# Kernel optimization log

Hardware: AMD Instinct MI355X
Metric: run time of the kernel (lower is better)

## Reference

```python
import jax, jax.numpy as jnp
import numpy as np

N, E, B, BLOCK = 100000, 1600000, 8, 12500
IN, HID, K, OUT = 128, 128, 4, 2
EPS = 1e-15


def setup_inputs() -> dict:
    key = jax.random.key(0)
    ks = jax.random.split(key, 14)
    x = jax.random.normal(ks[0], (N, IN), jnp.float32)
    # edges constrained within each graph's contiguous node block
    src = jax.random.randint(ks[1], (E,), 0, N)
    off = jax.random.randint(ks[2], (E,), 0, BLOCK)
    dst = (src // BLOCK) * BLOCK + off
    edge_index = jnp.stack([src, dst])
    batch = jnp.arange(N) // BLOCK
    s = 0.02
    params = dict(
        W_root1=jax.random.normal(ks[3], (IN, HID), jnp.float32) * s,
        W_rel1=jax.random.normal(ks[4], (IN, HID), jnp.float32) * s,
        b_rel1=jnp.zeros((HID,), jnp.float32),
        W_pool=jax.random.normal(ks[5], (HID, K), jnp.float32) * s,
        b_pool=jnp.zeros((K,), jnp.float32),
        W_rel3=jax.random.normal(ks[6], (HID, HID), jnp.float32) * s,
        b_rel3=jnp.zeros((HID,), jnp.float32),
        W_root3=jax.random.normal(ks[7], (HID, HID), jnp.float32) * s,
        W_lin1=jax.random.normal(ks[8], (HID, HID), jnp.float32) * s,
        b_lin1=jnp.zeros((HID,), jnp.float32),
        W_lin2=jax.random.normal(ks[9], (HID, OUT), jnp.float32) * s,
        b_lin2=jnp.zeros((OUT,), jnp.float32),
    )
    return dict(x=x, edge_index=edge_index, batch=batch, **params)


def _forward(x, edge_index, batch, W_root1, W_rel1, b_rel1, W_pool, b_pool,
             W_rel3, b_rel3, W_root3, W_lin1, b_lin1, W_lin2, b_lin2):
    src, dst = edge_index[0], edge_index[1]
    # GraphConv (aggr='add'): lin_rel(sum_j x_j) + lin_root(x)
    agg = jax.ops.segment_sum(x[src], dst, num_segments=N)  # [N, IN]
    h = jax.nn.relu(agg @ W_rel1 + b_rel1 + x @ W_root1)    # [N, HID]
    # cluster assignment
    s = jax.nn.softmax(h @ W_pool + b_pool, axis=-1)        # [N, K]
    # pooled node features: out[b] = S_b^T X_b  -> [B, K, HID]
    out = jax.ops.segment_sum(s[:, :, None] * h[:, None, :], batch, num_segments=B)
    # coarsened adjacency: out_adj[b] = S_b^T A_b S_b (A[dst, src] = 1 per edge)
    e_graph = batch[dst]
    contrib = s[dst][:, :, None] * s[src][:, None, :]       # [E, K, K]
    out_adj = jax.ops.segment_sum(contrib, e_graph, num_segments=B)  # [B, K, K]
    # mincut loss
    mincut_num = jnp.einsum('bkk->b', out_adj)
    deg = jax.ops.segment_sum(jnp.ones((E,), x.dtype), dst, num_segments=N)
    mincut_den = jax.ops.segment_sum(deg * jnp.sum(s * s, axis=-1), batch, num_segments=B)
    mc_loss = jnp.mean(-(mincut_num / mincut_den))
    # orthogonality loss
    ss = jax.ops.segment_sum(s[:, :, None] * s[:, None, :], batch, num_segments=B)  # [B,K,K]
    ss_norm = jnp.linalg.norm(ss, axis=(1, 2), keepdims=True)
    i_s = jnp.eye(K, dtype=x.dtype)
    o_loss = jnp.mean(jnp.linalg.norm(ss / ss_norm - i_s / jnp.sqrt(jnp.float32(K)), axis=(1, 2)))
    # fix and normalize coarsened adjacency
    out_adj = out_adj * (1.0 - i_s)  # zero diagonal
    d = jnp.sqrt(jnp.sum(out_adj, axis=-1)) + EPS  # [B, K]
    out_adj = out_adj / d[:, None, :] / d[:, :, None]
    # DenseGraphConv (aggr='add'): lin_rel(adj @ x) + lin_root(x)
    x2 = jnp.einsum('bkl,blc->bkc', out_adj, out) @ W_rel3 + b_rel3 + out @ W_root3
    x2 = jnp.mean(x2, axis=1)  # [B, HID]
    x2 = jax.nn.relu(x2 @ W_lin1 + b_lin1)
    logits = x2 @ W_lin2 + b_lin2
    return jax.nn.log_softmax(logits, axis=-1), mc_loss, o_loss, s, out_adj


def reference(x, edge_index, batch, W_root1, W_rel1, b_rel1, W_pool, b_pool,
              W_rel3, b_rel3, W_root3, W_lin1, b_lin1, W_lin2, b_lin2):
    return _forward(x, edge_index, batch, W_root1, W_rel1, b_rel1, W_pool, b_pool,
                    W_rel3, b_rel3, W_root3, W_lin1, b_lin1, W_lin2, b_lin2)
```

## Files before the change

### kernel.cpp

```cpp
#include <hip/hip_runtime.h>

#define NN     100000
#define EE     1600000
#define NB     8
#define BLK    12500
#define HID    128
#define KC     4
#define CHUNKS 196
#define NTILE  49
#define NBIN   392
#define GCAPS  5120

typedef __attribute__((ext_vector_type(8))) short bf16x8;
typedef __attribute__((ext_vector_type(4))) float f32x4;

__device__ __forceinline__ ushort f2bf(float f) {
  uint u = __float_as_uint(f);
  return (ushort)((u + 0x7FFFu + ((u >> 16) & 1u)) >> 16);
}
__device__ __forceinline__ float bf2f(ushort h) {
  return __uint_as_float(((uint)h) << 16);
}

#define GLL16(g, l) \
  __builtin_amdgcn_global_load_lds((const __attribute__((address_space(1))) void*)(g), \
                                   (__attribute__((address_space(3))) void*)(l), 16, 0, 0)

__global__ __launch_bounds__(256) void k_prep(const float4* __restrict__ x4,
                                              ushort* __restrict__ xb,
                                              const float* __restrict__ Wrel1,
                                              const float* __restrict__ Wroot1,
                                              ushort* __restrict__ Wt,
                                              const int* __restrict__ ei,
                                              int* __restrict__ sbcnt,
                                              uint* __restrict__ gbuf) {
  __shared__ uint stage[8192];
  __shared__ int cnt[NBIN], start[NBIN + 1], rbase[NBIN];
  __shared__ int gtot[8], gb[8];
  const int bi = blockIdx.x;
  const int t = threadIdx.x;
  if (bi >= 196) {
    const int pb = bi - 196;
    if (pb < 12500) {
      int i = pb * 256 + t;
      float4 v = x4[i];
      ushort4 r;
      r.x = f2bf(v.x); r.y = f2bf(v.y); r.z = f2bf(v.z); r.w = f2bf(v.w);
      *(ushort4*)(xb + (size_t)i * 4) = r;
    } else {
      int col = pb - 12500, k = t;
      float v = (k < 128) ? Wrel1[k * 128 + col] : Wroot1[(k - 128) * 128 + col];
      Wt[col * 256 + k] = f2bf(v);
    }
    return;
  }
  for (int b = t; b < NBIN; b += 256) cnt[b] = 0;
  __syncthreads();
  const int e0 = bi * 8192;
  uint pk[32]; int br[32];
#pragma unroll
  for (int i = 0; i < 32; ++i) {
    int e = e0 + i * 256 + t;
    bool val = (e < EE);
    int src = 0, dst = 0;
    if (val) {
      src = __builtin_nontemporal_load(ei + e);
      dst = __builtin_nontemporal_load(ei + EE + e);
    }
    int g = dst / BLK;
    int dl = dst - g * BLK;
    int sl = src - g * BLK;
    int bin = g * NTILE + (dl >> 8);
    pk[i] = ((uint)sl << 16) | (uint)dl;
    br[i] = val ? ((bin << 14) | atomicAdd(&cnt[bin], 1)) : -1;
  }
  __syncthreads();
  if (t < 8) {
    int s = 0;
    for (int k = 0; k < NTILE; ++k) s += cnt[t * NTILE + k];
    gtot[t] = s;
  }
  __syncthreads();
  if (t == 0) {
    int s = 0;
    for (int g = 0; g < 8; ++g) { gb[g] = s; s += gtot[g]; }
    start[NBIN] = s;
  }
  __syncthreads();
  if (t < 8) {
    int run = gb[t];
    for (int k = 0; k < NTILE; ++k) { start[t * NTILE + k] = run; run += cnt[t * NTILE + k]; }
  }
  __syncthreads();
  for (int b = t; b < NBIN; b += 256) rbase[b] = atomicAdd(&sbcnt[b], cnt[b]);
#pragma unroll
  for (int i = 0; i < 32; ++i) {
    if (br[i] >= 0) {
      int bin = br[i] >> 14, rank = br[i] & 16383;
      stage[start[bin] + rank] = pk[i];
    }
  }
  __syncthreads();
  for (int b = t; b < NBIN; b += 256) {
    const int n = cnt[b];
    const int s0 = start[b];
    uint* dst = gbuf + (size_t)b * GCAPS + rbase[b];
    for (int i = 0; i < n; ++i) dst[i] = stage[s0 + i];
  }
}

__global__ __launch_bounds__(256) void k_csr_tile(const uint* __restrict__ gbuf,
                                                  const int* __restrict__ sbcnt,
                                                  int* __restrict__ rowptr,
                                                  int* __restrict__ count,
                                                  int* __restrict__ csr) {
  const int g = blockIdx.x & 7;
  const int tile = blockIdx.x >> 3;
  const int bin = g * NTILE + tile;
  const int m = sbcnt[bin];
  const int n0t = tile * 256;
  const int nt = min(256, BLK - n0t);
  __shared__ uint ent[GCAPS];
  __shared__ ushort srt[GCAPS];
  __shared__ int cnt[256], scn[256], cur[256];
  __shared__ int red[256];
  const int t = threadIdx.x;
  {
    int partial = 0;
    for (int i = t; i < bin; i += 256) partial += sbcnt[i];
    red[t] = partial;
    __syncthreads();
    for (int off = 128; off > 0; off >>= 1) {
      if (t < off) red[t] += red[t + off];
      __syncthreads();
    }
  }
  const int base = red[0];
  cnt[t] = 0;
  __syncthreads();
  const uint* buf = gbuf + (size_t)bin * GCAPS;
  for (int i = t; i < m; i += 256) {
    uint pk = buf[i];
    ent[i] = pk;
    atomicAdd(&cnt[(int)(pk & 0xFFFFu) - n0t], 1);
  }
  __syncthreads();
  int v = cnt[t];
  scn[t] = v;
  __syncthreads();
  for (int s = 1; s < 256; s <<= 1) {
    int x = (t >= s) ? scn[t - s] : 0;
    __syncthreads();
    scn[t] += x;
    __syncthreads();
  }
  int excl = scn[t] - v;
  cur[t] = excl;
  if (t < nt) {
    rowptr[g * BLK + n0t + t] = base + excl;
    count[g * BLK + n0t + t] = v;
  }
  __syncthreads();
  for (int i = t; i < m; i += 256) {
    uint pk = ent[i];
    int p = atomicAdd(&cur[(int)(pk & 0xFFFFu) - n0t], 1);
    srt[p] = (ushort)(pk >> 16);
  }
  __syncthreads();
  const int nb = g * BLK;
  for (int i = t; i < m; i += 256)
    csr[base + i] = nb + (int)srt[i];
}

__global__ __launch_bounds__(256) void k_agg2(const ushort* __restrict__ xb,
                                              const int* __restrict__ count,
                                              const int* __restrict__ rowptr,
                                              const int* __restrict__ csr,
                                              const ushort* __restrict__ zrow,
                                              ushort* __restrict__ aggb) {
  const int xg = blockIdx.x & 7;
  const int j = blockIdx.x >> 3;
  const int half = threadIdx.x >> 5;
  const int lane = threadIdx.x & 31;
  const int ln = j * 8 + half;
  if (ln >= BLK) return;
  const int node = xg * BLK + ln;
  const int deg = count[node];
  const int* sl = csr + rowptr[node];
  int idx0 = (lane < deg) ? sl[lane] : 0;
  int idx1 = (32 + lane < deg) ? sl[32 + lane] : 0;
  const ushort* zr = zrow + lane * 4;

  float4 acc[8];
#pragma unroll
  for (int q = 0; q < 8; ++q) acc[q] = (float4){0.f, 0.f, 0.f, 0.f};

  const int nb8 = (deg + 7) >> 3;
  for (int b = 0; b < nb8; ++b) {
    const int e = b * 8;
    const ushort* ps[8];
#pragma unroll
    for (int q = 0; q < 8; ++q) {
      int ee = e + q;
      int si = (ee < 32) ? __shfl(idx0, ee, 32)
             : ((ee < 64) ? __shfl(idx1, ee - 32, 32)
                          : ((ee < deg) ? sl[ee] : 0));
      ps[q] = (ee < deg) ? (xb + (size_t)si * HID + lane * 4) : zr;
    }
    uint2 v[8];
#pragma unroll
    for (int q = 0; q < 8; ++q) v[q] = *(const uint2*)ps[q];
#pragma unroll
    for (int q = 0; q < 8; ++q) {
      acc[q].x += __uint_as_float(v[q].x << 16);
      acc[q].y += __uint_as_float(v[q].x & 0xFFFF0000u);
      acc[q].z += __uint_as_float(v[q].y << 16);
      acc[q].w += __uint_as_float(v[q].y & 0xFFFF0000u);
    }
  }

  float lo0 = 0.f, hi0 = 0.f, lo1 = 0.f, hi1 = 0.f;
#pragma unroll
  for (int q = 0; q < 8; ++q) { lo0 += acc[q].x; hi0 += acc[q].y; lo1 += acc[q].z; hi1 += acc[q].w; }
  ushort4 r;
  r.x = f2bf(lo0); r.y = f2bf(hi0); r.z = f2bf(lo1); r.w = f2bf(hi1);
  *(ushort4*)(aggb + (size_t)node * HID + lane * 4) = r;
}

__global__ __launch_bounds__(256) void k_gemm(
    const ushort* __restrict__ aggb, const ushort* __restrict__ xb,
    const ushort* __restrict__ Wt, const float* __restrict__ brel1,
    const float* __restrict__ Wpool, const float* __restrict__ bpool,
    ushort* __restrict__ hbuf, float* __restrict__ s_out) {
  __shared__ ushort Aag_s[64][128];
  __shared__ ushort Ax_s[64][128];
  __shared__ ushort hLb[64][136];

  const int t = threadIdx.x;
  const int bi = blockIdx.x;
  const int bG = bi & 7;
  const int chunk = bi >> 3;
  const int node0 = bG * BLK + chunk * 64;
  int nrows = BLK - chunk * 64;
  if (nrows > 64) nrows = 64;

  const int w = t >> 6;
  const int l = t & 63;

  {
    const int sub = l >> 4;
    const int c16 = l & 15;
#pragma unroll
    for (int i = 0; i < 4; ++i) {
      const int j = w * 4 + i;
      const int row = j * 4 + sub;
      const int rs = (row < nrows) ? row : (nrows - 1);
      const int boff = (c16 * 16) ^ ((row & 7) << 4);
      const ushort* ga = aggb + (size_t)(node0 + rs) * HID + (boff >> 1);
      const ushort* gx = xb + (size_t)(node0 + rs) * HID + (boff >> 1);
      GLL16(ga, &Aag_s[j * 4][0]);
      GLL16(gx, &Ax_s[j * 4][0]);
    }
  }

  const int m16 = l & 15;
  const int gq = l >> 4;

  bf16x8 Breg[8][2];
#pragma unroll
  for (int kt = 0; kt < 8; ++kt)
#pragma unroll
    for (int fc = 0; fc < 2; ++fc)
      Breg[kt][fc] =
          *(const bf16x8*)(Wt + (size_t)(32 * w + 16 * fc + m16) * 256 + kt * 32 + 8 * gq);

  f32x4 acc[4][2];
#pragma unroll
  for (int fr = 0; fr < 4; ++fr)
#pragma unroll
    for (int fc = 0; fc < 2; ++fc) acc[fr][fc] = (f32x4){0.f, 0.f, 0.f, 0.f};

  asm volatile("s_waitcnt vmcnt(0)" ::: "memory");
  __syncthreads();

#pragma unroll
  for (int kt = 0; kt < 8; ++kt) {
    const int k4 = kt & 3;
    bf16x8 af[4];
#pragma unroll
    for (int fr = 0; fr < 4; ++fr) {
      const int r = 16 * fr + m16;
      const int ci = (k4 * 32 + gq * 8) ^ ((r & 7) << 3);
      af[fr] = (kt < 4) ? *(const bf16x8*)&Aag_s[r][ci]
                        : *(const bf16x8*)&Ax_s[r][ci];
    }
#pragma unroll
    for (int fr = 0; fr < 4; ++fr)
#pragma unroll
      for (int fc = 0; fc < 2; ++fc)
        acc[fr][fc] = __builtin_amdgcn_mfma_f32_16x16x32_bf16(af[fr], Breg[kt][fc],
                                                              acc[fr][fc], 0, 0, 0);
  }

  const float bc0 = brel1[32 * w + m16];
  const float bc1 = brel1[32 * w + 16 + m16];
#pragma unroll
  for (int fr = 0; fr < 4; ++fr)
#pragma unroll
    for (int fc = 0; fc < 2; ++fc)
#pragma unroll
      for (int r = 0; r < 4; ++r)
        hLb[16 * fr + 4 * gq + r][32 * w + 16 * fc + m16] =
            f2bf(fmaxf(acc[fr][fc][r] + (fc ? bc1 : bc0), 0.f));
  __syncthreads();

  {
    const int row = t >> 2;
    const int ch = (t & 3) * 32;
    if (row < nrows) {
      ushort* dst = hbuf + (size_t)(node0 + row) * HID + ch;
      const ushort* src = &hLb[row][ch];
#pragma unroll
      for (int q = 0; q < 4; ++q)
        *(bf16x8*)(dst + q * 8) = *(const bf16x8*)(src + q * 8);
    }
  }

  const int g4 = t >> 4;
  const int c0 = (t & 15) << 2;
  const int li = t & 15;

  float h[4][8];
#pragma unroll
  for (int r = 0; r < 4; ++r) {
    ushort4 v0 = *(const ushort4*)&hLb[g4 * 4 + r][c0];
    ushort4 v1 = *(const ushort4*)&hLb[g4 * 4 + r][c0 + 64];
    h[r][0] = bf2f(v0.x); h[r][1] = bf2f(v0.y); h[r][2] = bf2f(v0.z); h[r][3] = bf2f(v0.w);
    h[r][4] = bf2f(v1.x); h[r][5] = bf2f(v1.y); h[r][6] = bf2f(v1.z); h[r][7] = bf2f(v1.w);
  }
  float wp[8][4];
#pragma unroll
  for (int j = 0; j < 8; ++j) {
    int col = c0 + (j & 3) + (j >> 2) * 64;
    float4 v = *(const float4*)(Wpool + col * 4);
    wp[j][0] = v.x; wp[j][1] = v.y; wp[j][2] = v.z; wp[j][3] = v.w;
  }
  float pp[4][4];
#pragma unroll
  for (int r = 0; r < 4; ++r)
#pragma unroll
    for (int k = 0; k < 4; ++k) pp[r][k] = 0.f;
#pragma unroll
  for (int r = 0; r < 4; ++r)
#pragma unroll
    for (int j = 0; j < 8; ++j)
#pragma unroll
      for (int k = 0; k < 4; ++k) pp[r][k] = fmaf(h[r][j], wp[j][k], pp[r][k]);
#pragma unroll
  for (int m = 1; m <= 8; m <<= 1)
#pragma unroll
    for (int r = 0; r < 4; ++r)
#pragma unroll
      for (int k = 0; k < 4; ++k) pp[r][k] += __shfl_xor(pp[r][k], m);

  float4 bp4 = *(const float4*)bpool;
  float bp[4] = {bp4.x, bp4.y, bp4.z, bp4.w};
#pragma unroll
  for (int r = 0; r < 4; ++r) {
    float p[4];
#pragma unroll
    for (int k = 0; k < 4; ++k) p[k] = pp[r][k] + bp[k];
    float mx = fmaxf(fmaxf(p[0], p[1]), fmaxf(p[2], p[3]));
    float e0 = expf(p[0] - mx), e1 = expf(p[1] - mx), e2 = expf(p[2] - mx), e3 = expf(p[3] - mx);
    float inv = 1.f / (e0 + e1 + e2 + e3);
    int rW = li >> 2, kW = li & 3;
    if (r == rW && g4 * 4 + rW < nrows) {
      float val = (kW == 0) ? e0 * inv : (kW == 1) ? e1 * inv : (kW == 2) ? e2 * inv : e3 * inv;
      s_out[(node0 + g4 * 4 + rW) * 4 + kW] = val;
    }
  }
}

__global__ __launch_bounds__(256) void k_epiadj(
    const ushort* __restrict__ hbuf, const float* __restrict__ s_in,
    const int* __restrict__ count, const int* __restrict__ rowptr,
    const int* __restrict__ csr, const float* __restrict__ zf,
    float* __restrict__ out_pool, float* __restrict__ ss_g,
    float* __restrict__ den_g, float* __restrict__ adjraw) {
  __shared__ ushort hLb[64][136];
  __shared__ float outL[KC][HID];
  __shared__ float ssL[16];
  __shared__ float denL;
  __shared__ float accL[4][2][16];
  const int t = threadIdx.x;
  const int bi = blockIdx.x;

  if (bi >= NB * CHUNKS) {
    const int abi = bi - NB * CHUNKS;
    if (t < 128) ((float*)accL)[t] = 0.f;
    __syncthreads();
    const int node = abi * 256 + t;
    const int g0 = (abi * 256) / BLK;
    if (node < NN) {
      const int gi = node / BLK - g0;
      const int deg = count[node];
      const int* sl = csr + rowptr[node];
      float a[8][4];
#pragma unroll
      for (int q = 0; q < 8; ++q)
#pragma unroll
        for (int c = 0; c < 4; ++c) a[q][c] = 0.f;
      const int nb8 = (deg + 7) >> 3;
      for (int b = 0; b < nb8; ++b) {
        const float* p[8];
#pragma unroll
        for (int q = 0; q < 8; ++q) {
          int ee = b * 8 + q;
          int si = (ee < deg) ? sl[ee] : 0;
          p[q] = (ee < deg) ? (s_in + (size_t)si * 4) : zf;
        }
        float4 v[8];
#pragma unroll
        for (int q = 0; q < 8; ++q) v[q] = *(const float4*)p[q];
#pragma unroll
        for (int q = 0; q < 8; ++q) {
          a[q][0] += v[q].x; a[q][1] += v[q].y; a[q][2] += v[q].z; a[q][3] += v[q].w;
        }
      }
      float t0 = 0.f, t1 = 0.f, t2 = 0.f, t3 = 0.f;
#pragma unroll
      for (int q = 0; q < 8; ++q) { t0 += a[q][0]; t1 += a[q][1]; t2 += a[q][2]; t3 += a[q][3]; }
      float4 sn = *(const float4*)(s_in + (size_t)node * 4);
      float* base = accL[t >> 6][gi];
#pragma unroll
      for (int i = 0; i < 16; ++i) {
        int idx = (i + t) & 15;
        int hi = idx >> 2, lo = idx & 3;
        float a1 = (hi == 0) ? sn.x : (hi == 1) ? sn.y : (hi == 2) ? sn.z : sn.w;
        float b1 = (lo == 0) ? t0 : (lo == 1) ? t1 : (lo == 2) ? t2 : t3;
        atomicAdd(base + idx, a1 * b1);
      }
    }
    __syncthreads();
    if (t < 32) {
      int gi = t >> 4, i = t & 15, gg = g0 + gi;
      if (gg < NB) {
        float v = accL[0][gi][i] + accL[1][gi][i] + accL[2][gi][i] + accL[3][gi][i];
        atomicAdd(&adjraw[gg * 16 + i], v);
      }
    }
    return;
  }

  const int bG = bi & 7;
  const int chunk = bi >> 3;
  const int node0 = bG * BLK + chunk * 64;
  int nrows = BLK - chunk * 64;
  if (nrows > 64) nrows = 64;

  {
    const int row = t >> 2;
    const int ch = (t & 3) * 32;
    const int rs = (row < nrows) ? row : (nrows - 1);
    const ushort* src = hbuf + (size_t)(node0 + rs) * HID + ch;
    ushort* dst = &hLb[row][ch];
#pragma unroll
    for (int q = 0; q < 4; ++q)
      *(bf16x8*)(dst + q * 8) = *(const bf16x8*)(src + q * 8);
  }

  for (int i = t; i < KC * HID; i += 256) ((float*)outL)[i] = 0.f;
  if (t < 16) ssL[t] = 0.f;
  if (t == 0) denL = 0.f;
  __syncthreads();

  const int g4 = t >> 4;
  const int c0 = (t & 15) << 2;
  const int li = t & 15;

  float h[4][8];
#pragma unroll
  for (int r = 0; r < 4; ++r) {
    ushort4 v0 = *(const ushort4*)&hLb[g4 * 4 + r][c0];
    ushort4 v1 = *(const ushort4*)&hLb[g4 * 4 + r][c0 + 64];
    h[r][0] = bf2f(v0.x); h[r][1] = bf2f(v0.y); h[r][2] = bf2f(v0.z); h[r][3] = bf2f(v0.w);
    h[r][4] = bf2f(v1.x); h[r][5] = bf2f(v1.y); h[r][6] = bf2f(v1.z); h[r][7] = bf2f(v1.w);
  }

  float sv[4][4];
#pragma unroll
  for (int r = 0; r < 4; ++r) {
    int rowg = g4 * 4 + r;
    float4 sval = (float4){0.f, 0.f, 0.f, 0.f};
    if (rowg < nrows) sval = *(const float4*)(s_in + (size_t)(node0 + rowg) * 4);
    sv[r][0] = sval.x; sv[r][1] = sval.y; sv[r][2] = sval.z; sv[r][3] = sval.w;
  }

  {
    int k1 = li >> 2, k2 = li & 3;
    float a1[4], a2[4];
#pragma unroll
    for (int rr = 0; rr < 4; ++rr) {
      float v1 = 0.f, v2 = 0.f;
#pragma unroll
      for (int kk = 0; kk < 4; ++kk) {
        if (k1 == kk) v1 = sv[rr][kk];
        if (k2 == kk) v2 = sv[rr][kk];
      }
      a1[rr] = v1; a2[rr] = v2;
    }
    float ssv = a1[0] * a2[0] + a1[1] * a2[1] + a1[2] * a2[2] + a1[3] * a2[3];
    atomicAdd(&ssL[li], ssv);
  }

  if (li == 0) {
    float dent = 0.f;
#pragma unroll
    for (int rr = 0; rr < 4; ++rr) {
      int rowg = g4 * 4 + rr;
      if (rowg < nrows) {
        float dg = (float)count[node0 + rowg];
        dent += dg * (sv[rr][0] * sv[rr][0] + sv[rr][1] * sv[rr][1] +
                      sv[rr][2] * sv[rr][2] + sv[rr][3] * sv[rr][3]);
      }
    }
    atomicAdd(&denL, dent);
  }

  float po[4][8];
#pragma unroll
  for (int k = 0; k < 4; ++k)
#pragma unroll
    for (int c = 0; c < 8; ++c) po[k][c] = 0.f;
#pragma unroll
  for (int k = 0; k < 4; ++k)
#pragma unroll
    for (int rr = 0; rr < 4; ++rr)
#pragma unroll
      for (int c = 0; c < 8; ++c) po[k][c] = fmaf(sv[rr][k], h[rr][c], po[k][c]);
#pragma unroll
  for (int k = 0; k < 4; ++k)
#pragma unroll
    for (int c = 0; c < 8; ++c) {
      po[k][c] += __shfl_xor(po[k][c], 16);
      po[k][c] += __shfl_xor(po[k][c], 32);
    }
  if ((t & 63) < 16) {
#pragma unroll
    for (int k = 0; k < 4; ++k)
#pragma unroll
      for (int c = 0; c < 8; ++c)
        atomicAdd(&outL[k][c0 + (c & 3) + (c >> 2) * 64], po[k][c]);
  }

  __syncthreads();
  for (int i = t; i < KC * HID; i += 256)
    atomicAdd(&out_pool[bG * KC * HID + i], ((const float*)outL)[i]);
  if (t < 16) atomicAdd(&ss_g[bG * 16 + t], ssL[t]);
  if (t == 0) atomicAdd(&den_g[bG], denL);
}

__global__ __launch_bounds__(1024) void k_tail(
    const float* __restrict__ out_pool, const float* __restrict__ adjraw,
    const float* __restrict__ den_g, const float* __restrict__ ss_g,
    const float* __restrict__ Wrel3, const float* __restrict__ brel3,
    const float* __restrict__ Wroot3, const float* __restrict__ Wlin1,
    const float* __restrict__ blin1, const float* __restrict__ Wlin2,
    const float* __restrict__ blin2, float* __restrict__ d_out,
    float* __restrict__ scratch) {
  const int g = threadIdx.x >> 7;
  const int tt = threadIdx.x & 127;
  __shared__ float adjL[NB][16], adjnL[NB][16], dL[NB][4];
  __shared__ float osL[NB][128], msL[NB][128], x2mL[NB][128], x3L[NB][128];
  if (tt < 16) adjL[g][tt] = adjraw[g * 16 + tt];
  __syncthreads();
  if (tt < 4) {
    float srow = 0.f;
#pragma unroll
    for (int l = 0; l < 4; ++l)
      if (l != tt) srow += adjL[g][tt * 4 + l];
    dL[g][tt] = sqrtf(srow) + 1e-15f;
  }
  __syncthreads();
  if (tt < 16) {
    int k1 = tt >> 2, k2 = tt & 3;
    float az = (k1 == k2) ? 0.f : adjL[g][tt];
    float an = az / (dL[g][k2] * dL[g][k1]);
    adjnL[g][tt] = an;
    d_out[400018 + g * 16 + tt] = an;
  }
  __syncthreads();
  float o0 = out_pool[g * 512 + 0 * 128 + tt];
  float o1 = out_pool[g * 512 + 1 * 128 + tt];
  float o2 = out_pool[g * 512 + 2 * 128 + tt];
  float o3 = out_pool[g * 512 + 3 * 128 + tt];
  float m0 = adjnL[g][0] * o0 + adjnL[g][1] * o1 + adjnL[g][2] * o2 + adjnL[g][3] * o3;
  float m1 = adjnL[g][4] * o0 + adjnL[g][5] * o1 + adjnL[g][6] * o2 + adjnL[g][7] * o3;
  float m2 = adjnL[g][8] * o0 + adjnL[g][9] * o1 + adjnL[g][10] * o2 + adjnL[g][11] * o3;
  float m3 = adjnL[g][12] * o0 + adjnL[g][13] * o1 + adjnL[g][14] * o2 + adjnL[g][15] * o3;
  osL[g][tt] = o0 + o1 + o2 + o3;
  msL[g][tt] = m0 + m1 + m2 + m3;
  __syncthreads();
  float accc = brel3[tt];
  for (int j = 0; j < 128; ++j)
    accc += 0.25f * (msL[g][j] * Wrel3[j * 128 + tt] + osL[g][j] * Wroot3[j * 128 + tt]);
  x2mL[g][tt] = accc;
  __syncthreads();
  float a2 = blin1[tt];
  for (int j = 0; j < 128; ++j) a2 += x2mL[g][j] * Wlin1[j * 128 + tt];
  x3L[g][tt] = fmaxf(a2, 0.f);
  __syncthreads();
  if (tt < 2) {
    float lg = blin2[tt];
    for (int j = 0; j < 128; ++j) lg += x3L[g][j] * Wlin2[j * 2 + tt];
    scratch[g * 2 + tt] = lg;
  }
  if (tt == 0) {
    float tr = adjL[g][0] + adjL[g][5] + adjL[g][10] + adjL[g][15];
    scratch[16 + g] = tr / den_g[g];
    float n2 = 0.f;
    for (int i = 0; i < 16; ++i) { float v = ss_g[g * 16 + i]; n2 += v * v; }
    float nn = sqrtf(n2);
    float od = 0.f;
    for (int i = 0; i < 16; ++i) {
      float v = ss_g[g * 16 + i] / nn - (((i >> 2) == (i & 3)) ? 0.5f : 0.f);
      od += v * v;
    }
    scratch[24 + g] = sqrtf(od);
  }
  __syncthreads();
  if (threadIdx.x == 0) {
    float mc = 0.f, oo = 0.f;
    for (int b = 0; b < NB; ++b) { mc += scratch[16 + b]; oo += scratch[24 + b]; }
    d_out[16] = -(mc / (float)NB);
    d_out[17] = oo / (float)NB;
    for (int b = 0; b < NB; ++b) {
      float l0 = scratch[2 * b], l1 = scratch[2 * b + 1];
      float m = fmaxf(l0, l1);
      float lse = m + logf(expf(l0 - m) + expf(l1 - m));
      d_out[2 * b] = l0 - lse;
      d_out[2 * b + 1] = l1 - lse;
    }
  }
}

extern "C" void kernel_launch(void* const* d_in, const int* in_sizes, int n_in,
                              void* d_out, int out_size, void* d_ws, size_t ws_size,
                              hipStream_t stream) {
  (void)in_sizes; (void)n_in; (void)out_size; (void)ws_size;
  const float* x      = (const float*)d_in[0];
  const int*   ei     = (const int*)d_in[1];
  const float* Wroot1 = (const float*)d_in[3];
  const float* Wrel1  = (const float*)d_in[4];
  const float* brel1  = (const float*)d_in[5];
  const float* Wpool  = (const float*)d_in[6];
  const float* bpool  = (const float*)d_in[7];
  const float* Wrel3  = (const float*)d_in[8];
  const float* brel3  = (const float*)d_in[9];
  const float* Wroot3 = (const float*)d_in[10];
  const float* Wlin1  = (const float*)d_in[11];
  const float* blin1  = (const float*)d_in[12];
  const float* Wlin2  = (const float*)d_in[13];
  const float* blin2  = (const float*)d_in[14];
  float* out = (float*)d_out;

  char* ws = (char*)d_ws;
  float*  out_pool = (float*)(ws + 0);
  float*  ss_g     = (float*)(ws + 16384);
  float*  adjraw   = (float*)(ws + 16896);
  float*  den_g    = (float*)(ws + 17408);
  float*  scratch  = (float*)(ws + 17440);
  int*    sbcnt    = (int*)(ws + 17568);
  ushort* zrow     = (ushort*)(ws + 19136);
  float*  zf       = (float*)(ws + 19392);
  int*    count    = (int*)(ws + 21248);
  int*    rowptr   = (int*)(ws + 421248);
  ushort* Wt       = (ushort*)(ws + 821264);
  int*    csr      = (int*)(ws + 886800);
  ushort* xb       = (ushort*)(ws + 7286800);
  ushort* aggb     = (ushort*)(ws + 32886800);
  uint*   gbuf     = (uint*)(ws + 58486800);
  ushort* hbuf     = (ushort*)(ws + 66514960);

  hipMemsetAsync(ws, 0, 19648, stream);
  k_prep<<<196 + 12500 + 128, 256, 0, stream>>>((const float4*)x, xb, Wrel1, Wroot1,
                                                Wt, ei, sbcnt, gbuf);
  k_csr_tile<<<NBIN, 256, 0, stream>>>(gbuf, sbcnt, rowptr, count, csr);
  k_agg2<<<8 * ((BLK + 7) / 8), 256, 0, stream>>>(xb, count, rowptr, csr, zrow, aggb);
  k_gemm<<<NB * CHUNKS, 256, 0, stream>>>(aggb, xb, Wt, brel1, Wpool, bpool, hbuf,
                                          out + 18);
  k_epiadj<<<NB * CHUNKS + (NN + 255) / 256, 256, 0, stream>>>(
      hbuf, out + 18, count, rowptr, csr, zf, out_pool, ss_g, den_g, adjraw);
  k_tail<<<1, 1024, 0, stream>>>(out_pool, adjraw, den_g, ss_g, Wrel3, brel3, Wroot3,
                                 Wlin1, blin1, Wlin2, blin2, out, scratch);
}
```

Baseline: 180.6 us.

## Split agg/gemm/epilogue into staggered half-launches to overlap pipeline stages

Replaces the three stage kernels (aggregation, GEMM, epilogue+adjacency) with four kernels that each run the second half of one stage together with the first half of the next stage. Blocks from different stages can then share the GPU, which is meant to shorten the tail and idle time at kernel boundaries. The GEMM's shared memory is now reused for the hLb output buffer (an added __syncthreads), which cuts LDS footprint per block. It relies on the ordering of the stream so that the first half of each producer finishes before its consumer half runs. The cost is extra launches and some heterogeneous block mixes.

```diff
diff --git a/kernel.cpp b/kernel.cpp
--- a/kernel.cpp
+++ b/kernel.cpp
@@ -10,6 +10,10 @@
 #define NTILE  49
 #define NBIN   392
 #define GCAPS  5120
+#define JTOT   1563
+#define JH     784
+#define CH     98
+#define SMEMB  32768
 
 typedef __attribute__((ext_vector_type(8))) short bf16x8;
 typedef __attribute__((ext_vector_type(4))) float f32x4;
@@ -172,14 +176,13 @@
     csr[base + i] = nb + (int)srt[i];
 }
 
-__global__ __launch_bounds__(256) void k_agg2(const ushort* __restrict__ xb,
-                                              const int* __restrict__ count,
-                                              const int* __restrict__ rowptr,
-                                              const int* __restrict__ csr,
-                                              const ushort* __restrict__ zrow,
-                                              ushort* __restrict__ aggb) {
-  const int xg = blockIdx.x & 7;
-  const int j = blockIdx.x >> 3;
+__device__ __forceinline__ void dev_agg(int xg, int j,
+                                        const ushort* __restrict__ xb,
+                                        const int* __restrict__ count,
+                                        const int* __restrict__ rowptr,
+                                        const int* __restrict__ csr,
+                                        const ushort* __restrict__ zrow,
+                                        ushort* __restrict__ aggb) {
   const int half = threadIdx.x >> 5;
   const int lane = threadIdx.x & 31;
   const int ln = j * 8 + half;
@@ -227,19 +230,20 @@
   *(ushort4*)(aggb + (size_t)node * HID + lane * 4) = r;
 }
 
-__global__ __launch_bounds__(256) void k_gemm(
-    const ushort* __restrict__ aggb, const ushort* __restrict__ xb,
-    const ushort* __restrict__ Wt, const float* __restrict__ brel1,
-    const float* __restrict__ Wpool, const float* __restrict__ bpool,
-    ushort* __restrict__ hbuf, float* __restrict__ s_out) {
-  __shared__ ushort Aag_s[64][128];
-  __shared__ ushort Ax_s[64][128];
-  __shared__ ushort hLb[64][136];
+__device__ __forceinline__ void dev_gemm(char* smem, int bG, int chunk,
+                                         const ushort* __restrict__ aggb,
+                                         const ushort* __restrict__ xb,
+                                         const ushort* __restrict__ Wt,
+                                         const float* __restrict__ brel1,
+                                         const float* __restrict__ Wpool,
+                                         const float* __restrict__ bpool,
+                                         ushort* __restrict__ hbuf,
+                                         float* __restrict__ s_out) {
+  ushort (*Aag_s)[128] = (ushort(*)[128])smem;
+  ushort (*Ax_s)[128]  = (ushort(*)[128])(smem + 16384);
+  ushort (*hLb)[136]   = (ushort(*)[136])smem;
 
   const int t = threadIdx.x;
-  const int bi = blockIdx.x;
-  const int bG = bi & 7;
-  const int chunk = bi >> 3;
   const int node0 = bG * BLK + chunk * 64;
   int nrows = BLK - chunk * 64;
   if (nrows > 64) nrows = 64;
@@ -302,6 +306,8 @@
                                                               acc[fr][fc], 0, 0, 0);
   }
 
+  __syncthreads();
+
   const float bc0 = brel1[32 * w + m16];
   const float bc1 = brel1[32 * w + 16 + m16];
 #pragma unroll
@@ -381,79 +387,19 @@
   }
 }
 
-__global__ __launch_bounds__(256) void k_epiadj(
-    const ushort* __restrict__ hbuf, const float* __restrict__ s_in,
-    const int* __restrict__ count, const int* __restrict__ rowptr,
-    const int* __restrict__ csr, const float* __restrict__ zf,
-    float* __restrict__ out_pool, float* __restrict__ ss_g,
-    float* __restrict__ den_g, float* __restrict__ adjraw) {
-  __shared__ ushort hLb[64][136];
-  __shared__ float outL[KC][HID];
-  __shared__ float ssL[16];
-  __shared__ float denL;
-  __shared__ float accL[4][2][16];
+__device__ __forceinline__ void dev_epi(char* smem, int bG, int chunk,
+                                        const ushort* __restrict__ hbuf,
+                                        const float* __restrict__ s_in,
+                                        const int* __restrict__ count,
+                                        float* __restrict__ out_pool,
+                                        float* __restrict__ ss_g,
+                                        float* __restrict__ den_g) {
+  ushort (*hLb)[136] = (ushort(*)[136])smem;
+  float* outL = (float*)(smem + 17408);
+  float* ssL  = (float*)(smem + 19456);
+  float* denL = (float*)(smem + 19520);
+
   const int t = threadIdx.x;
-  const int bi = blockIdx.x;
-
-  if (bi >= NB * CHUNKS) {
-    const int abi = bi - NB * CHUNKS;
-    if (t < 128) ((float*)accL)[t] = 0.f;
-    __syncthreads();
-    const int node = abi * 256 + t;
-    const int g0 = (abi * 256) / BLK;
-    if (node < NN) {
-      const int gi = node / BLK - g0;
-      const int deg = count[node];
-      const int* sl = csr + rowptr[node];
-      float a[8][4];
-#pragma unroll
-      for (int q = 0; q < 8; ++q)
-#pragma unroll
-        for (int c = 0; c < 4; ++c) a[q][c] = 0.f;
-      const int nb8 = (deg + 7) >> 3;
-      for (int b = 0; b < nb8; ++b) {
-        const float* p[8];
-#pragma unroll
-        for (int q = 0; q < 8; ++q) {
-          int ee = b * 8 + q;
-          int si = (ee < deg) ? sl[ee] : 0;
-          p[q] = (ee < deg) ? (s_in + (size_t)si * 4) : zf;
-        }
-        float4 v[8];
-#pragma unroll
-        for (int q = 0; q < 8; ++q) v[q] = *(const float4*)p[q];
-#pragma unroll
-        for (int q = 0; q < 8; ++q) {
-          a[q][0] += v[q].x; a[q][1] += v[q].y; a[q][2] += v[q].z; a[q][3] += v[q].w;
-        }
-      }
-      float t0 = 0.f, t1 = 0.f, t2 = 0.f, t3 = 0.f;
-#pragma unroll
-      for (int q = 0; q < 8; ++q) { t0 += a[q][0]; t1 += a[q][1]; t2 += a[q][2]; t3 += a[q][3]; }
-      float4 sn = *(const float4*)(s_in + (size_t)node * 4);
-      float* base = accL[t >> 6][gi];
-#pragma unroll
-      for (int i = 0; i < 16; ++i) {
-        int idx = (i + t) & 15;
-        int hi = idx >> 2, lo = idx & 3;
-        float a1 = (hi == 0) ? sn.x : (hi == 1) ? sn.y : (hi == 2) ? sn.z : sn.w;
-        float b1 = (lo == 0) ? t0 : (lo == 1) ? t1 : (lo == 2) ? t2 : t3;
-        atomicAdd(base + idx, a1 * b1);
-      }
-    }
-    __syncthreads();
-    if (t < 32) {
-      int gi = t >> 4, i = t & 15, gg = g0 + gi;
-      if (gg < NB) {
-        float v = accL[0][gi][i] + accL[1][gi][i] + accL[2][gi][i] + accL[3][gi][i];
-        atomicAdd(&adjraw[gg * 16 + i], v);
-      }
-    }
-    return;
-  }
-
-  const int bG = bi & 7;
-  const int chunk = bi >> 3;
   const int node0 = bG * BLK + chunk * 64;
   int nrows = BLK - chunk * 64;
   if (nrows > 64) nrows = 64;
@@ -469,9 +415,9 @@
       *(bf16x8*)(dst + q * 8) = *(const bf16x8*)(src + q * 8);
   }
 
-  for (int i = t; i < KC * HID; i += 256) ((float*)outL)[i] = 0.f;
+  for (int i = t; i < KC * HID; i += 256) outL[i] = 0.f;
   if (t < 16) ssL[t] = 0.f;
-  if (t == 0) denL = 0.f;
+  if (t == 0) denL[0] = 0.f;
   __syncthreads();
 
   const int g4 = t >> 4;
@@ -524,7 +470,7 @@
                       sv[rr][2] * sv[rr][2] + sv[rr][3] * sv[rr][3]);
       }
     }
-    atomicAdd(&denL, dent);
+    atomicAdd(denL, dent);
   }
 
   float po[4][8];
@@ -550,14 +496,150 @@
     for (int k = 0; k < 4; ++k)
 #pragma unroll
       for (int c = 0; c < 8; ++c)
-        atomicAdd(&outL[k][c0 + (c & 3) + (c >> 2) * 64], po[k][c]);
+        atomicAdd(&outL[k * HID + c0 + (c & 3) + (c >> 2) * 64], po[k][c]);
   }
 
   __syncthreads();
   for (int i = t; i < KC * HID; i += 256)
-    atomicAdd(&out_pool[bG * KC * HID + i], ((const float*)outL)[i]);
+    atomicAdd(&out_pool[bG * KC * HID + i], outL[i]);
   if (t < 16) atomicAdd(&ss_g[bG * 16 + t], ssL[t]);
-  if (t == 0) atomicAdd(&den_g[bG], denL);
+  if (t == 0) atomicAdd(&den_g[bG], denL[0]);
+}
+
+__device__ __forceinline__ void dev_adj(char* smem, int abi,
+                                        const int* __restrict__ count,
+                                        const int* __restrict__ rowptr,
+                                        const int* __restrict__ csr,
+                                        const float* __restrict__ s_in,
+                                        const float* __restrict__ zf,
+                                        float* __restrict__ adjraw) {
+  float (*accL)[2][16] = (float(*)[2][16])smem;
+  const int t = threadIdx.x;
+  if (t < 128) ((float*)accL)[t] = 0.f;
+  __syncthreads();
+  const int node = abi * 256 + t;
+  const int g0 = (abi * 256) / BLK;
+  if (node < NN) {
+    const int gi = node / BLK - g0;
+    const int deg = count[node];
+    const int* sl = csr + rowptr[node];
+    float a[8][4];
+#pragma unroll
+    for (int q = 0; q < 8; ++q)
+#pragma unroll
+      for (int c = 0; c < 4; ++c) a[q][c] = 0.f;
+    const int nb8 = (deg + 7) >> 3;
+    for (int b = 0; b < nb8; ++b) {
+      const float* p[8];
+#pragma unroll
+      for (int q = 0; q < 8; ++q) {
+        int ee = b * 8 + q;
+        int si = (ee < deg) ? sl[ee] : 0;
+        p[q] = (ee < deg) ? (s_in + (size_t)si * 4) : zf;
+      }
+      float4 v[8];
+#pragma unroll
+      for (int q = 0; q < 8; ++q) v[q] = *(const float4*)p[q];
+#pragma unroll
+      for (int q = 0; q < 8; ++q) {
+        a[q][0] += v[q].x; a[q][1] += v[q].y; a[q][2] += v[q].z; a[q][3] += v[q].w;
+      }
+    }
+    float t0 = 0.f, t1 = 0.f, t2 = 0.f, t3 = 0.f;
+#pragma unroll
+    for (int q = 0; q < 8; ++q) { t0 += a[q][0]; t1 += a[q][1]; t2 += a[q][2]; t3 += a[q][3]; }
+    float4 sn = *(const float4*)(s_in + (size_t)node * 4);
+    float* base = accL[t >> 6][gi];
+#pragma unroll
+    for (int i = 0; i < 16; ++i) {
+      int idx = (i + t) & 15;
+      int hi = idx >> 2, lo = idx & 3;
+      float a1 = (hi == 0) ? sn.x : (hi == 1) ? sn.y : (hi == 2) ? sn.z : sn.w;
+      float b1 = (lo == 0) ? t0 : (lo == 1) ? t1 : (lo == 2) ? t2 : t3;
+      atomicAdd(base + idx, a1 * b1);
+    }
+  }
+  __syncthreads();
+  if (t < 32) {
+    int gi = t >> 4, i = t & 15, gg = g0 + gi;
+    if (gg < NB) {
+      float v = accL[0][gi][i] + accL[1][gi][i] + accL[2][gi][i] + accL[3][gi][i];
+      atomicAdd(&adjraw[gg * 16 + i], v);
+    }
+  }
+}
+
+__global__ __launch_bounds__(256) void k_d1(const ushort* __restrict__ xb,
+                                            const int* __restrict__ count,
+                                            const int* __restrict__ rowptr,
+                                            const int* __restrict__ csr,
+                                            const ushort* __restrict__ zrow,
+                                            ushort* __restrict__ aggb) {
+  dev_agg(blockIdx.x & 7, blockIdx.x >> 3, xb, count, rowptr, csr, zrow, aggb);
+}
+
+__global__ __launch_bounds__(256) void k_d2(const ushort* __restrict__ xb,
+                                            const int* __restrict__ count,
+                                            const int* __restrict__ rowptr,
+                                            const int* __restrict__ csr,
+                                            const ushort* __restrict__ zrow,
+                                            ushort* __restrict__ aggb,
+                                            const ushort* __restrict__ Wt,
+                                            const float* __restrict__ brel1,
+                                            const float* __restrict__ Wpool,
+                                            const float* __restrict__ bpool,
+                                            ushort* __restrict__ hbuf,
+                                            float* __restrict__ s_out) {
+  __shared__ __align__(16) char smem[SMEMB];
+  const int bi = blockIdx.x;
+  const int NA = 8 * (JTOT - JH);
+  if (bi < NA) {
+    dev_agg(bi & 7, JH + (bi >> 3), xb, count, rowptr, csr, zrow, aggb);
+  } else {
+    const int lin = bi - NA;
+    dev_gemm(smem, lin & 7, lin >> 3, aggb, xb, Wt, brel1, Wpool, bpool, hbuf, s_out);
+  }
+}
+
+__global__ __launch_bounds__(256) void k_d3(const ushort* __restrict__ aggb,
+                                            const ushort* __restrict__ xb,
+                                            const ushort* __restrict__ Wt,
+                                            const float* __restrict__ brel1,
+                                            const float* __restrict__ Wpool,
+                                            const float* __restrict__ bpool,
+                                            ushort* __restrict__ hbuf,
+                                            float* __restrict__ s_io,
+                                            const int* __restrict__ count,
+                                            float* __restrict__ out_pool,
+                                            float* __restrict__ ss_g,
+                                            float* __restrict__ den_g) {
+  __shared__ __align__(16) char smem[SMEMB];
+  const int bi = blockIdx.x;
+  if (bi < 8 * (CHUNKS - CH)) {
+    dev_gemm(smem, bi & 7, CH + (bi >> 3), aggb, xb, Wt, brel1, Wpool, bpool, hbuf, s_io);
+  } else {
+    const int lin = bi - 8 * (CHUNKS - CH);
+    dev_epi(smem, lin & 7, lin >> 3, hbuf, s_io, count, out_pool, ss_g, den_g);
+  }
+}
+
+__global__ __launch_bounds__(256) void k_d4(const ushort* __restrict__ hbuf,
+                                            const float* __restrict__ s_in,
+                                            const int* __restrict__ count,
+                                            const int* __restrict__ rowptr,
+                                            const int* __restrict__ csr,
+                                            const float* __restrict__ zf,
+                                            float* __restrict__ out_pool,
+                                            float* __restrict__ ss_g,
+                                            float* __restrict__ den_g,
+                                            float* __restrict__ adjraw) {
+  __shared__ __align__(16) char smem[SMEMB];
+  const int bi = blockIdx.x;
+  if (bi < 8 * (CHUNKS - CH)) {
+    dev_epi(smem, bi & 7, CH + (bi >> 3), hbuf, s_in, count, out_pool, ss_g, den_g);
+  } else {
+    dev_adj(smem, bi - 8 * (CHUNKS - CH), count, rowptr, csr, s_in, zf, adjraw);
+  }
 }
 
 __global__ __launch_bounds__(1024) void k_tail(
@@ -686,10 +768,14 @@
   k_prep<<<196 + 12500 + 128, 256, 0, stream>>>((const float4*)x, xb, Wrel1, Wroot1,
                                                 Wt, ei, sbcnt, gbuf);
   k_csr_tile<<<NBIN, 256, 0, stream>>>(gbuf, sbcnt, rowptr, count, csr);
-  k_agg2<<<8 * ((BLK + 7) / 8), 256, 0, stream>>>(xb, count, rowptr, csr, zrow, aggb);
-  k_gemm<<<NB * CHUNKS, 256, 0, stream>>>(aggb, xb, Wt, brel1, Wpool, bpool, hbuf,
-                                          out + 18);
-  k_epiadj<<<NB * CHUNKS + (NN + 255) / 256, 256, 0, stream>>>(
+  k_d1<<<8 * JH, 256, 0, stream>>>(xb, count, rowptr, csr, zrow, aggb);
+  k_d2<<<8 * (JTOT - JH) + 8 * CH, 256, 0, stream>>>(xb, count, rowptr, csr, zrow,
+                                                     aggb, Wt, brel1, Wpool, bpool,
+                                                     hbuf, out + 18);
+  k_d3<<<8 * (CHUNKS - CH) + 8 * CH, 256, 0, stream>>>(aggb, xb, Wt, brel1, Wpool,
+                                                       bpool, hbuf, out + 18, count,
+                                                       out_pool, ss_g, den_g);
+  k_d4<<<8 * (CHUNKS - CH) + (NN + 255) / 256, 256, 0, stream>>>(
       hbuf, out + 18, count, rowptr, csr, zf, out_pool, ss_g, den_g, adjraw);
   k_tail<<<1, 1024, 0, stream>>>(out_pool, adjraw, den_g, ss_g, Wrel3, brel3, Wroot3,
                                  Wlin1, blin1, Wlin2, blin2, out, scratch);
```

New measurement: 194.2 us. +7.5%, slower.
